# Performance work log

Hardware: AMD Instinct MI355X
Metric: run time of the kernel (lower is better)

## Reference

```python
import jax, jax.numpy as jnp
import numpy as np

N_NODES = 100000
NFEAT = 256
NHID = 8
HEADS = 8
NCLASS = 32
N_EDGES = 1600000
NEG_SLOPE = 0.2


def setup_inputs() -> dict:
    key = jax.random.key(0)
    ks = jax.random.split(key, 10)
    glorot = lambda k, shape: jax.random.uniform(
        k, shape, jnp.float32, -1.0, 1.0) * np.sqrt(6.0 / (shape[0] + shape[-1]))
    x = jax.random.normal(ks[0], (N_NODES, NFEAT), jnp.float32)
    edge_index = jax.random.randint(ks[1], (2, N_EDGES), 0, N_NODES, jnp.int64)
    W1 = glorot(ks[2], (NFEAT, HEADS * NHID))
    a_src1 = glorot(ks[3], (HEADS, NHID))
    a_dst1 = glorot(ks[4], (HEADS, NHID))
    b1 = jnp.zeros((HEADS * NHID,), jnp.float32)
    W2 = glorot(ks[5], (HEADS * NHID, NCLASS))
    a_src2 = glorot(ks[6], (1, NCLASS))
    a_dst2 = glorot(ks[7], (1, NCLASS))
    b2 = jnp.zeros((NCLASS,), jnp.float32)
    return {"x": x, "edge_index": edge_index, "W1": W1, "a_src1": a_src1,
            "a_dst1": a_dst1, "b1": b1, "W2": W2, "a_src2": a_src2,
            "a_dst2": a_dst2, "b2": b2}


def gat_conv(x, src, dst, W, a_src, a_dst, b, heads, ch, concat):
    """One PyG-style GATConv layer (eval mode, self-loops already in src/dst)."""
    n = x.shape[0]
    h = (x @ W).reshape(n, heads, ch)                      # [N,H,C]
    al_s = jnp.einsum('nhc,hc->nh', h, a_src)              # [N,H]
    al_d = jnp.einsum('nhc,hc->nh', h, a_dst)              # [N,H]
    e = al_s[src] + al_d[dst]                              # [E,H]
    e = jnp.where(e >= 0, e, NEG_SLOPE * e)                # LeakyReLU(0.2)
    # segment softmax over destination node (self-loops => no empty segments)
    m = jax.ops.segment_max(e, dst, num_segments=n)
    e = jnp.exp(e - m[dst])
    s = jax.ops.segment_sum(e, dst, num_segments=n)
    alpha = e / (s[dst] + 1e-16)                           # [E,H]
    msg = h[src] * alpha[:, :, None]                       # [E,H,C]
    out = jax.ops.segment_sum(msg, dst, num_segments=n)    # [N,H,C]
    out = out.reshape(n, heads * ch) if concat else out.mean(axis=1)
    return out + b


def reference(x, edge_index, W1, a_src1, a_dst1, b1, W2, a_src2, a_dst2, b2):
    n = x.shape[0]
    loop = jnp.arange(n, dtype=edge_index.dtype)
    src = jnp.concatenate([edge_index[0], loop])
    dst = jnp.concatenate([edge_index[1], loop])
    h = gat_conv(x, src, dst, W1, a_src1, a_dst1, b1, HEADS, NHID, True)
    h = jax.nn.elu(h)
    out = gat_conv(h, src, dst, W2, a_src2, a_dst2, b2, 1, NCLASS, False)
    return jax.nn.log_softmax(out, axis=1)
```

## Files before the change

### kernel.cpp

```cpp
#include <hip/hip_runtime.h>
#include <math.h>

#define N_NODES 100000
#define NFEAT 256
#define D1 64
#define HEADS 8
#define NHID 8
#define NCLASS 32
#define NUM_EDGES 1600000
#define E_TOT 1700000
#define NEG_SLOPE 0.2f

#define BSHIFT 8
#define NBUCK 391
#define BCAP 5120
#define BIN_EPB 4096
#define BIN_EPT 16


#define OFF_H1    0
#define OFF_OUT1  6400000
#define OFF_ALS1  12800000
#define OFF_ALD1  13600000
#define OFF_ALS2  14400000
#define OFF_ALD2  14500000
#define OFF_BCUR  14600000
#define OFF_ROWP  14601024
#define OFF_CNT   14701024
#define OFF_BIN   14801024
#define OFF_CSR   16802944

typedef __attribute__((ext_vector_type(8))) short bf16x8;
typedef __attribute__((ext_vector_type(4))) float f32x4;

__device__ __forceinline__ float lrelu(float x) { return x >= 0.f ? x : NEG_SLOPE * x; }

__device__ __forceinline__ unsigned f32_to_bf16_rne(float f) {
    unsigned u = __float_as_uint(f);
    return (u + 0x7fffu + ((u >> 16) & 1u)) >> 16;
}
__device__ __forceinline__ unsigned pack_bf16x2(float lo, float hi) {
    return f32_to_bf16_rne(lo) | (f32_to_bf16_rne(hi) << 16);
}
__device__ __forceinline__ float2 unpack_bf16x2(unsigned v) {
    return make_float2(__uint_as_float(v << 16), __uint_as_float(v & 0xffff0000u));
}

__device__ __forceinline__ void edge_src_dst(const int* __restrict__ ei, int e, int& src, int& dst) {
    if (e < NUM_EDGES) { src = ei[e]; dst = ei[NUM_EDGES + e]; }
    else { src = e - NUM_EDGES; dst = e - NUM_EDGES; }
}

__global__ __launch_bounds__(256) void gemm1_kernel(const float* __restrict__ x,
                                                    const float* __restrict__ W1,
                                                    const float* __restrict__ a_src,
                                                    const float* __restrict__ a_dst,
                                                    ushort* __restrict__ h1u,
                                                    float* __restrict__ als,
                                                    float* __restrict__ ald) {
    __shared__ unsigned xbf[2][64 * 20];
    const int tid = threadIdx.x;
    const int wv = tid >> 6;
    const int l = tid & 63;
    const int lm = l & 15;
    const int quad = l >> 4;
    const int r0 = blockIdx.x * 64;

    bf16x8 bfrag[8];
#pragma unroll
    for (int kb = 0; kb < 8; kb++)
#pragma unroll
        for (int j = 0; j < 8; j++) {
            const int k = kb * 32 + quad * 8 + j;
            bfrag[kb][j] = (short)f32_to_bf16_rne(W1[k * D1 + wv * 16 + lm]);
        }

    f32x4 acc[4];
#pragma unroll
    for (int s = 0; s < 4; s++) acc[s] = (f32x4)(0.f);

    const int sr = tid >> 2;
    const int sk = (tid & 3) * 8;
    const bool rok = (r0 + sr) < N_NODES;
    const float* xrow = &x[(size_t)(r0 + sr) * NFEAT];
    const int swrd = sr * 20 + (tid & 3) * 4;

    {
        uint4 pv = make_uint4(0, 0, 0, 0);
        if (rok) {
            const float4 va = *(const float4*)&xrow[sk];
            const float4 vb = *(const float4*)&xrow[sk + 4];
            pv.x = pack_bf16x2(va.x, va.y);
            pv.y = pack_bf16x2(va.z, va.w);
            pv.z = pack_bf16x2(vb.x, vb.y);
            pv.w = pack_bf16x2(vb.z, vb.w);
        }
        *(uint4*)&xbf[0][swrd] = pv;
    }
    __syncthreads();

#pragma unroll
    for (int kb = 0; kb < 8; kb++) {
        const int cur = kb & 1;
        const int nxt = cur ^ 1;
        float4 na = make_float4(0.f, 0.f, 0.f, 0.f);
        float4 nb = make_float4(0.f, 0.f, 0.f, 0.f);
        if (kb < 7 && rok) {
            na = *(const float4*)&xrow[(kb + 1) * 32 + sk];
            nb = *(const float4*)&xrow[(kb + 1) * 32 + sk + 4];
        }
#pragma unroll
        for (int s = 0; s < 4; s++) {
            const uint4 u = *(const uint4*)&xbf[cur][(s * 16 + lm) * 20 + quad * 4];
            const bf16x8 af = *(const bf16x8*)&u;
            acc[s] = __builtin_amdgcn_mfma_f32_16x16x32_bf16(af, bfrag[kb], acc[s], 0, 0, 0);
        }
        if (kb < 7) {
            uint4 pv;
            pv.x = pack_bf16x2(na.x, na.y);
            pv.y = pack_bf16x2(na.z, na.w);
            pv.z = pack_bf16x2(nb.x, nb.y);
            pv.w = pack_bf16x2(nb.z, nb.w);
            *(uint4*)&xbf[nxt][swrd] = pv;
            __syncthreads();
        }
    }

    const int head = wv * 2 + (lm >> 3);
    const int jc = l & 7;
    const float asl = a_src[head * NHID + jc];
    const float adl = a_dst[head * NHID + jc];
    const int col = wv * 16 + lm;
#pragma unroll
    for (int s = 0; s < 4; s++) {
#pragma unroll
        for (int r = 0; r < 4; r++) {
            const int row = r0 + s * 16 + quad * 4 + r;
            const float v = acc[s][r];
            float ps = v * asl, pd = v * adl;
            ps += __shfl_xor(ps, 1, 64); pd += __shfl_xor(pd, 1, 64);
            ps += __shfl_xor(ps, 2, 64); pd += __shfl_xor(pd, 2, 64);
            ps += __shfl_xor(ps, 4, 64); pd += __shfl_xor(pd, 4, 64);
            if (row < N_NODES) {
                h1u[(size_t)row * D1 + col] = (ushort)f32_to_bf16_rne(v);
                if (jc == 0) { als[row * HEADS + head] = ps; ald[row * HEADS + head] = pd; }
            }
        }
    }
}

__global__ __launch_bounds__(256) void bin_kernel(const int* __restrict__ ei,
                                                  int* __restrict__ bcur,
                                                  int* __restrict__ bin) {
    __shared__ int lcnt[NBUCK];
    __shared__ int lbase[NBUCK];
    const int tid = threadIdx.x;
    for (int b = tid; b < NBUCK; b += 256) lcnt[b] = 0;
    __syncthreads();
    const int e0 = blockIdx.x * BIN_EPB;
    int pk[BIN_EPT], bk[BIN_EPT], loff[BIN_EPT];
#pragma unroll
    for (int i = 0; i < BIN_EPT; i++) {
        const int e = e0 + i * 256 + tid;
        if (e < E_TOT) {
            int src, dst; edge_src_dst(ei, e, src, dst);
            bk[i] = dst >> BSHIFT;
            pk[i] = ((dst & 255) << 20) | src;
            loff[i] = atomicAdd(&lcnt[bk[i]], 1);
        } else bk[i] = -1;
    }
    __syncthreads();
    for (int b = tid; b < NBUCK; b += 256) {
        const int c = lcnt[b];
        lbase[b] = c ? atomicAdd(&bcur[b], c) : 0;
    }
    __syncthreads();
#pragma unroll
    for (int i = 0; i < BIN_EPT; i++) {
        if (bk[i] >= 0)
            bin[(size_t)bk[i] * BCAP + lbase[bk[i]] + loff[i]] = pk[i];
    }
}

__global__ __launch_bounds__(256) void bsort_kernel(const int* __restrict__ bcur,
                                                    const int* __restrict__ bin,
                                                    int* __restrict__ csr,
                                                    int* __restrict__ row_ptr,
                                                    int* __restrict__ cnt) {
    __shared__ int hcnt[256];
    __shared__ int hpre[256];
    __shared__ int cur[256];
    __shared__ int ssrc[BCAP];
    const int tid = threadIdx.x;
    const int bkt = blockIdx.x;
    const int cntb = bcur[bkt];
    const int base = bkt * BCAP;
    hcnt[tid] = 0;
    __syncthreads();
    for (int i = tid; i < cntb; i += 256)
        atomicAdd(&hcnt[bin[base + i] >> 20], 1);
    __syncthreads();
    const int myc = hcnt[tid];
    hpre[tid] = myc;
    __syncthreads();
    for (int off = 1; off < 256; off <<= 1) {
        const int t = (tid >= off) ? hpre[tid - off] : 0;
        __syncthreads();
        hpre[tid] += t;
        __syncthreads();
    }
    const int exc = hpre[tid] - myc;
    cur[tid] = exc;
    __syncthreads();
    for (int i = tid; i < cntb; i += 256) {
        const int v = bin[base + i];
        const int pos = atomicAdd(&cur[v >> 20], 1);
        ssrc[pos] = v & 0xFFFFF;
    }
    __syncthreads();
    for (int i = tid; i < cntb; i += 256) csr[base + i] = ssrc[i];
    const int n = (bkt << BSHIFT) + tid;
    if (n < N_NODES) { row_ptr[n] = base + exc; cnt[n] = myc; }
}

__global__ __launch_bounds__(256) void gather1_kernel(const int* __restrict__ row_ptr,
                                                      const int* __restrict__ cnt,
                                                      const int* __restrict__ csr_src,
                                                      const unsigned* __restrict__ h1b,
                                                      const float* __restrict__ als,
                                                      const float* __restrict__ ald,
                                                      float* __restrict__ out1) {
    const int tid = threadIdx.x;
    const int n = blockIdx.x * 4 + (tid >> 6);
    const int l = tid & 63;
    const int q = l >> 3;
    const int h = l & 7;
    const int start = row_ptr[n];
    const int deg = cnt[n];
    const float aldn = ald[n * HEADS + h];
    float a0 = 0.f, a1 = 0.f, a2 = 0.f, a3 = 0.f;
    float a4 = 0.f, a5 = 0.f, a6 = 0.f, a7 = 0.f, wsum = 0.f;

    int i = q;
    float e0 = 0.f, e1 = 0.f;
    uint4 u0 = make_uint4(0u, 0u, 0u, 0u);
    uint4 u1 = make_uint4(0u, 0u, 0u, 0u);
    int s2 = 0;
    if (i < deg) {
        const int s0 = csr_src[start + i];
        e0 = als[s0 * HEADS + h];
        u0 = *(const uint4*)&h1b[(size_t)s0 * 32 + h * 4];
    }
    if (i + 8 < deg) {
        const int s1 = csr_src[start + i + 8];
        e1 = als[s1 * HEADS + h];
        u1 = *(const uint4*)&h1b[(size_t)s1 * 32 + h * 4];
    }
    if (i + 16 < deg) s2 = csr_src[start + i + 16];

    for (; i < deg; i += 8) {
        int s3 = 0;
        if (i + 24 < deg) s3 = csr_src[start + i + 24];
        float e2 = 0.f;
        uint4 u2 = make_uint4(0u, 0u, 0u, 0u);
        if (i + 16 < deg) {
            e2 = als[s2 * HEADS + h];
            u2 = *(const uint4*)&h1b[(size_t)s2 * 32 + h * 4];
        }
        const float w = __expf(lrelu(e0 + aldn));
        const float2 p0 = unpack_bf16x2(u0.x);
        const float2 p1 = unpack_bf16x2(u0.y);
        const float2 p2 = unpack_bf16x2(u0.z);
        const float2 p3 = unpack_bf16x2(u0.w);
        a0 = fmaf(p0.x, w, a0); a1 = fmaf(p0.y, w, a1);
        a2 = fmaf(p1.x, w, a2); a3 = fmaf(p1.y, w, a3);
        a4 = fmaf(p2.x, w, a4); a5 = fmaf(p2.y, w, a5);
        a6 = fmaf(p3.x, w, a6); a7 = fmaf(p3.y, w, a7);
        wsum += w;
        e0 = e1; u0 = u1; e1 = e2; u1 = u2; s2 = s3;
    }

    a0 += __shfl_down(a0, 32, 64); a1 += __shfl_down(a1, 32, 64);
    a2 += __shfl_down(a2, 32, 64); a3 += __shfl_down(a3, 32, 64);
    a4 += __shfl_down(a4, 32, 64); a5 += __shfl_down(a5, 32, 64);
    a6 += __shfl_down(a6, 32, 64); a7 += __shfl_down(a7, 32, 64);
    wsum += __shfl_down(wsum, 32, 64);
    a0 += __shfl_down(a0, 16, 64); a1 += __shfl_down(a1, 16, 64);
    a2 += __shfl_down(a2, 16, 64); a3 += __shfl_down(a3, 16, 64);
    a4 += __shfl_down(a4, 16, 64); a5 += __shfl_down(a5, 16, 64);
    a6 += __shfl_down(a6, 16, 64); a7 += __shfl_down(a7, 16, 64);
    wsum += __shfl_down(wsum, 16, 64);
    a0 += __shfl_down(a0, 8, 64); a1 += __shfl_down(a1, 8, 64);
    a2 += __shfl_down(a2, 8, 64); a3 += __shfl_down(a3, 8, 64);
    a4 += __shfl_down(a4, 8, 64); a5 += __shfl_down(a5, 8, 64);
    a6 += __shfl_down(a6, 8, 64); a7 += __shfl_down(a7, 8, 64);
    wsum += __shfl_down(wsum, 8, 64);
    if (l < 8) {
        const float inv = 1.f / (wsum + 1e-16f);
        float* op = &out1[(size_t)n * D1 + h * 8];
        *(float4*)&op[0] = make_float4(a0 * inv, a1 * inv, a2 * inv, a3 * inv);
        *(float4*)&op[4] = make_float4(a4 * inv, a5 * inv, a6 * inv, a7 * inv);
    }
}

__global__ __launch_bounds__(256) void layer2_node_kernel(const float* __restrict__ out1,
                                                          const float* __restrict__ b1,
                                                          const float* __restrict__ W2,
                                                          const float* __restrict__ a_src2,
                                                          const float* __restrict__ a_dst2,
                                                          unsigned* __restrict__ h2b,
                                                          float* __restrict__ als2,
                                                          float* __restrict__ ald2) {
    __shared__ float w2l[D1 * NCLASS];
    __shared__ float b1l[D1];
    __shared__ float a2l[2 * NCLASS];
    const int tid = threadIdx.x;
    for (int i = tid; i < D1 * NCLASS; i += 256) w2l[i] = W2[i];
    if (tid < D1) b1l[tid] = b1[tid];
    if (tid < NCLASS) a2l[tid] = a_src2[tid];
    else if (tid < 2 * NCLASS) a2l[tid] = a_dst2[tid - NCLASS];
    __syncthreads();

    const int n = blockIdx.x * 256 + tid;
    if (n >= N_NODES) return;
    float acc[NCLASS];
#pragma unroll
    for (int c = 0; c < NCLASS; c++) acc[c] = 0.f;
    float as = 0.f, ad = 0.f;
    const float4* rp = (const float4*)&out1[(size_t)n * D1];
#pragma unroll 2
    for (int k4 = 0; k4 < 16; k4++) {
        const float4 v4 = rp[k4];
        const float vv[4] = {v4.x, v4.y, v4.z, v4.w};
#pragma unroll
        for (int j = 0; j < 4; j++) {
            const int k = k4 * 4 + j;
            float z = vv[j] + b1l[k];
            z = z > 0.f ? z : expm1f(z);
            const float* wr = &w2l[k * NCLASS];
#pragma unroll
            for (int c = 0; c < NCLASS; c++) acc[c] += z * wr[c];
        }
    }
#pragma unroll
    for (int c = 0; c < NCLASS; c++) { as += acc[c] * a2l[c]; ad += acc[c] * a2l[NCLASS + c]; }
#pragma unroll
    for (int q = 0; q < 4; q++) {
        uint4 pv;
        pv.x = pack_bf16x2(acc[q * 8 + 0], acc[q * 8 + 1]);
        pv.y = pack_bf16x2(acc[q * 8 + 2], acc[q * 8 + 3]);
        pv.z = pack_bf16x2(acc[q * 8 + 4], acc[q * 8 + 5]);
        pv.w = pack_bf16x2(acc[q * 8 + 6], acc[q * 8 + 7]);
        *(uint4*)&h2b[(size_t)n * 16 + q * 4] = pv;
    }
    als2[n] = as; ald2[n] = ad;
}

__global__ __launch_bounds__(256) void gather2_kernel(const int* __restrict__ row_ptr,
                                                      const int* __restrict__ cnt,
                                                      const int* __restrict__ csr_src,
                                                      const unsigned* __restrict__ h2b,
                                                      const float* __restrict__ als2,
                                                      const float* __restrict__ ald2,
                                                      float* __restrict__ out2) {
    const int tid = threadIdx.x;
    const int n = blockIdx.x * 4 + (tid >> 6);
    const int l = tid & 63;
    const int q = l >> 2;
    const int c = l & 3;
    const int start = row_ptr[n];
    const int deg = cnt[n];
    const float aldn = ald2[n];
    float a0 = 0.f, a1 = 0.f, a2 = 0.f, a3 = 0.f;
    float a4 = 0.f, a5 = 0.f, a6 = 0.f, a7 = 0.f, wsum = 0.f;

    int i = q;
    float e0 = 0.f, e1 = 0.f;
    uint4 u0 = make_uint4(0u, 0u, 0u, 0u);
    uint4 u1 = make_uint4(0u, 0u, 0u, 0u);
    int s2 = 0;
    if (i < deg) {
        const int s0 = csr_src[start + i];
        e0 = als2[s0];
        u0 = *(const uint4*)&h2b[(size_t)s0 * 16 + c * 4];
    }
    if (i + 16 < deg) {
        const int s1 = csr_src[start + i + 16];
        e1 = als2[s1];
        u1 = *(const uint4*)&h2b[(size_t)s1 * 16 + c * 4];
    }
    if (i + 32 < deg) s2 = csr_src[start + i + 32];

    for (; i < deg; i += 16) {
        int s3 = 0;
        if (i + 48 < deg) s3 = csr_src[start + i + 48];
        float e2 = 0.f;
        uint4 u2 = make_uint4(0u, 0u, 0u, 0u);
        if (i + 32 < deg) {
            e2 = als2[s2];
            u2 = *(const uint4*)&h2b[(size_t)s2 * 16 + c * 4];
        }
        const float w = __expf(lrelu(e0 + aldn));
        const float2 p0 = unpack_bf16x2(u0.x);
        const float2 p1 = unpack_bf16x2(u0.y);
        const float2 p2 = unpack_bf16x2(u0.z);
        const float2 p3 = unpack_bf16x2(u0.w);
        a0 = fmaf(p0.x, w, a0); a1 = fmaf(p0.y, w, a1);
        a2 = fmaf(p1.x, w, a2); a3 = fmaf(p1.y, w, a3);
        a4 = fmaf(p2.x, w, a4); a5 = fmaf(p2.y, w, a5);
        a6 = fmaf(p3.x, w, a6); a7 = fmaf(p3.y, w, a7);
        wsum += w;
        e0 = e1; u0 = u1; e1 = e2; u1 = u2; s2 = s3;
    }

    a0 += __shfl_down(a0, 32, 64); a1 += __shfl_down(a1, 32, 64);
    a2 += __shfl_down(a2, 32, 64); a3 += __shfl_down(a3, 32, 64);
    a4 += __shfl_down(a4, 32, 64); a5 += __shfl_down(a5, 32, 64);
    a6 += __shfl_down(a6, 32, 64); a7 += __shfl_down(a7, 32, 64);
    wsum += __shfl_down(wsum, 32, 64);
    a0 += __shfl_down(a0, 16, 64); a1 += __shfl_down(a1, 16, 64);
    a2 += __shfl_down(a2, 16, 64); a3 += __shfl_down(a3, 16, 64);
    a4 += __shfl_down(a4, 16, 64); a5 += __shfl_down(a5, 16, 64);
    a6 += __shfl_down(a6, 16, 64); a7 += __shfl_down(a7, 16, 64);
    wsum += __shfl_down(wsum, 16, 64);
    a0 += __shfl_down(a0, 8, 64); a1 += __shfl_down(a1, 8, 64);
    a2 += __shfl_down(a2, 8, 64); a3 += __shfl_down(a3, 8, 64);
    a4 += __shfl_down(a4, 8, 64); a5 += __shfl_down(a5, 8, 64);
    a6 += __shfl_down(a6, 8, 64); a7 += __shfl_down(a7, 8, 64);
    wsum += __shfl_down(wsum, 8, 64);
    a0 += __shfl_down(a0, 4, 64); a1 += __shfl_down(a1, 4, 64);
    a2 += __shfl_down(a2, 4, 64); a3 += __shfl_down(a3, 4, 64);
    a4 += __shfl_down(a4, 4, 64); a5 += __shfl_down(a5, 4, 64);
    a6 += __shfl_down(a6, 4, 64); a7 += __shfl_down(a7, 4, 64);
    wsum += __shfl_down(wsum, 4, 64);
    if (l < 4) {
        const float inv = 1.f / (wsum + 1e-16f);
        float* op = &out2[(size_t)n * NCLASS + c * 8];
        *(float4*)&op[0] = make_float4(a0 * inv, a1 * inv, a2 * inv, a3 * inv);
        *(float4*)&op[4] = make_float4(a4 * inv, a5 * inv, a6 * inv, a7 * inv);
    }
}

__global__ __launch_bounds__(256) void logsoftmax_kernel(const float* __restrict__ out2,
                                                         const float* __restrict__ b2,
                                                         float* __restrict__ out) {
    __shared__ float b2l[NCLASS];
    if (threadIdx.x < NCLASS) b2l[threadIdx.x] = b2[threadIdx.x];
    __syncthreads();
    const int n = blockIdx.x * 256 + threadIdx.x;
    if (n >= N_NODES) return;
    float v[NCLASS];
    float mx = -INFINITY;
    const float4* rp = (const float4*)&out2[(size_t)n * NCLASS];
#pragma unroll
    for (int c4 = 0; c4 < NCLASS / 4; c4++) {
        const float4 t = rp[c4];
        v[c4 * 4 + 0] = t.x + b2l[c4 * 4 + 0];
        v[c4 * 4 + 1] = t.y + b2l[c4 * 4 + 1];
        v[c4 * 4 + 2] = t.z + b2l[c4 * 4 + 2];
        v[c4 * 4 + 3] = t.w + b2l[c4 * 4 + 3];
    }
#pragma unroll
    for (int c = 0; c < NCLASS; c++) mx = fmaxf(mx, v[c]);
    float s = 0.f;
#pragma unroll
    for (int c = 0; c < NCLASS; c++) s += __expf(v[c] - mx);
    const float lse = mx + logf(s);
    float4* op = (float4*)&out[(size_t)n * NCLASS];
#pragma unroll
    for (int c4 = 0; c4 < NCLASS / 4; c4++)
        op[c4] = make_float4(v[c4 * 4] - lse, v[c4 * 4 + 1] - lse, v[c4 * 4 + 2] - lse, v[c4 * 4 + 3] - lse);
}

extern "C" void kernel_launch(void* const* d_in, const int* in_sizes, int n_in,
                              void* d_out, int out_size, void* d_ws, size_t ws_size,
                              hipStream_t stream) {
    const float* x      = (const float*)d_in[0];
    const int*   ei     = (const int*)d_in[1];
    const float* W1     = (const float*)d_in[2];
    const float* a_src1 = (const float*)d_in[3];
    const float* a_dst1 = (const float*)d_in[4];
    const float* b1     = (const float*)d_in[5];
    const float* W2     = (const float*)d_in[6];
    const float* a_src2 = (const float*)d_in[7];
    const float* a_dst2 = (const float*)d_in[8];
    const float* b2     = (const float*)d_in[9];
    float* out = (float*)d_out;
    float* ws  = (float*)d_ws;

    ushort* h1u     = (ushort*)(ws + OFF_H1);
    unsigned* h1b   = (unsigned*)(ws + OFF_H1);
    float* out1     = ws + OFF_OUT1;
    float* als1     = ws + OFF_ALS1;
    float* ald1     = ws + OFF_ALD1;
    float* als2     = ws + OFF_ALS2;
    float* ald2     = ws + OFF_ALD2;
    int*   bcur     = (int*)(ws + OFF_BCUR);
    int*   row_ptr  = (int*)(ws + OFF_ROWP);
    int*   cnt      = (int*)(ws + OFF_CNT);
    int*   bin      = (int*)(ws + OFF_BIN);
    int*   csr      = (int*)(ws + OFF_CSR);
    unsigned* h2b   = (unsigned*)(ws + OFF_H1);
    float* out2     = ws + OFF_H1 + 3200000;

    hipMemsetAsync(bcur, 0, NBUCK * sizeof(int), stream);

    const int NB = (N_NODES + 255) / 256;

    gemm1_kernel<<<(N_NODES + 63) / 64, 256, 0, stream>>>(x, W1, a_src1, a_dst1, h1u, als1, ald1);
    bin_kernel<<<(E_TOT + BIN_EPB - 1) / BIN_EPB, 256, 0, stream>>>(ei, bcur, bin);
    bsort_kernel<<<NBUCK, 256, 0, stream>>>(bcur, bin, csr, row_ptr, cnt);
    gather1_kernel<<<N_NODES / 4, 256, 0, stream>>>(row_ptr, cnt, csr, h1b, als1, ald1, out1);
    layer2_node_kernel<<<NB, 256, 0, stream>>>(out1, b1, W2, a_src2, a_dst2, h2b, als2, ald2);
    gather2_kernel<<<N_NODES / 4, 256, 0, stream>>>(row_ptr, cnt, csr, h2b, als2, ald2, out2);
    logsoftmax_kernel<<<NB, 256, 0, stream>>>(out2, b2, out);
}
```

Measured before the change: 357.0 us.

## Fuse layer-2 node transform into gather1 and log-softmax into gather2

Folds the per-node ELU + W2 projection and attention-logit computation into the epilogue of the layer-1 aggregation kernel, using a shared-memory buffer per wavefront and W2 read from global memory. It also folds the bias add and log-softmax into the layer-2 aggregation epilogue using cross-lane shuffles. This removes two kernel launches and the round-trips of the out1 and out2 intermediates through global memory. In exchange, gather1 gains a block barrier and per-wave W2 reads, which may add latency to a gather-bound kernel. h2b moves to its own workspace region, so it no longer overlaps h1.

New measurement: 360.3 us. Within noise of the previous version (+0.9%).

```diff
diff --git a/kernel.cpp b/kernel.cpp
--- a/kernel.cpp
+++ b/kernel.cpp
@@ -19,7 +19,7 @@
 
 
 #define OFF_H1    0
-#define OFF_OUT1  6400000
+#define OFF_H2    6400000
 #define OFF_ALS1  12800000
 #define OFF_ALD1  13600000
 #define OFF_ALS2  14400000
@@ -229,9 +229,17 @@
                                                       const unsigned* __restrict__ h1b,
                                                       const float* __restrict__ als,
                                                       const float* __restrict__ ald,
-                                                      float* __restrict__ out1) {
+                                                      const float* __restrict__ b1,
+                                                      const float* __restrict__ W2,
+                                                      const float* __restrict__ a_src2,
+                                                      const float* __restrict__ a_dst2,
+                                                      unsigned* __restrict__ h2b,
+                                                      float* __restrict__ als2,
+                                                      float* __restrict__ ald2) {
+    __shared__ float zbuf[4][64];
     const int tid = threadIdx.x;
-    const int n = blockIdx.x * 4 + (tid >> 6);
+    const int wv = tid >> 6;
+    const int n = blockIdx.x * 4 + wv;
     const int l = tid & 63;
     const int q = l >> 3;
     const int h = l & 7;
@@ -295,65 +303,49 @@
     a4 += __shfl_down(a4, 8, 64); a5 += __shfl_down(a5, 8, 64);
     a6 += __shfl_down(a6, 8, 64); a7 += __shfl_down(a7, 8, 64);
     wsum += __shfl_down(wsum, 8, 64);
+
     if (l < 8) {
         const float inv = 1.f / (wsum + 1e-16f);
-        float* op = &out1[(size_t)n * D1 + h * 8];
-        *(float4*)&op[0] = make_float4(a0 * inv, a1 * inv, a2 * inv, a3 * inv);
-        *(float4*)&op[4] = make_float4(a4 * inv, a5 * inv, a6 * inv, a7 * inv);
-    }
-}
-
-__global__ __launch_bounds__(256) void layer2_node_kernel(const float* __restrict__ out1,
-                                                          const float* __restrict__ b1,
-                                                          const float* __restrict__ W2,
-                                                          const float* __restrict__ a_src2,
-                                                          const float* __restrict__ a_dst2,
-                                                          unsigned* __restrict__ h2b,
-                                                          float* __restrict__ als2,
-                                                          float* __restrict__ ald2) {
-    __shared__ float w2l[D1 * NCLASS];
-    __shared__ float b1l[D1];
-    __shared__ float a2l[2 * NCLASS];
-    const int tid = threadIdx.x;
-    for (int i = tid; i < D1 * NCLASS; i += 256) w2l[i] = W2[i];
-    if (tid < D1) b1l[tid] = b1[tid];
-    if (tid < NCLASS) a2l[tid] = a_src2[tid];
-    else if (tid < 2 * NCLASS) a2l[tid] = a_dst2[tid - NCLASS];
-    __syncthreads();
-
-    const int n = blockIdx.x * 256 + tid;
-    if (n >= N_NODES) return;
-    float acc[NCLASS];
-#pragma unroll
-    for (int c = 0; c < NCLASS; c++) acc[c] = 0.f;
-    float as = 0.f, ad = 0.f;
-    const float4* rp = (const float4*)&out1[(size_t)n * D1];
-#pragma unroll 2
-    for (int k4 = 0; k4 < 16; k4++) {
-        const float4 v4 = rp[k4];
-        const float vv[4] = {v4.x, v4.y, v4.z, v4.w};
-#pragma unroll
-        for (int j = 0; j < 4; j++) {
-            const int k = k4 * 4 + j;
-            float z = vv[j] + b1l[k];
-            z = z > 0.f ? z : expm1f(z);
-            const float* wr = &w2l[k * NCLASS];
-#pragma unroll
-            for (int c = 0; c < NCLASS; c++) acc[c] += z * wr[c];
-        }
-    }
-#pragma unroll
-    for (int c = 0; c < NCLASS; c++) { as += acc[c] * a2l[c]; ad += acc[c] * a2l[NCLASS + c]; }
-#pragma unroll
-    for (int q = 0; q < 4; q++) {
-        uint4 pv;
-        pv.x = pack_bf16x2(acc[q * 8 + 0], acc[q * 8 + 1]);
-        pv.y = pack_bf16x2(acc[q * 8 + 2], acc[q * 8 + 3]);
-        pv.z = pack_bf16x2(acc[q * 8 + 4], acc[q * 8 + 5]);
-        pv.w = pack_bf16x2(acc[q * 8 + 6], acc[q * 8 + 7]);
-        *(uint4*)&h2b[(size_t)n * 16 + q * 4] = pv;
-    }
-    als2[n] = as; ald2[n] = ad;
+        const float4 b1a = *(const float4*)&b1[l * 8];
+        const float4 b1b = *(const float4*)&b1[l * 8 + 4];
+        float z0 = a0 * inv + b1a.x; z0 = z0 > 0.f ? z0 : expm1f(z0);
+        float z1 = a1 * inv + b1a.y; z1 = z1 > 0.f ? z1 : expm1f(z1);
+        float z2 = a2 * inv + b1a.z; z2 = z2 > 0.f ? z2 : expm1f(z2);
+        float z3 = a3 * inv + b1a.w; z3 = z3 > 0.f ? z3 : expm1f(z3);
+        float z4 = a4 * inv + b1b.x; z4 = z4 > 0.f ? z4 : expm1f(z4);
+        float z5 = a5 * inv + b1b.y; z5 = z5 > 0.f ? z5 : expm1f(z5);
+        float z6 = a6 * inv + b1b.z; z6 = z6 > 0.f ? z6 : expm1f(z6);
+        float z7 = a7 * inv + b1b.w; z7 = z7 > 0.f ? z7 : expm1f(z7);
+        *(float4*)&zbuf[wv][l * 8]     = make_float4(z0, z1, z2, z3);
+        *(float4*)&zbuf[wv][l * 8 + 4] = make_float4(z4, z5, z6, z7);
+    }
+    __syncthreads();
+
+    const int c = l & 31;
+    const int kh = l >> 5;
+    float y = 0.f;
+    const float* wbase = &W2[(kh * 32) * NCLASS + c];
+#pragma unroll
+    for (int j4 = 0; j4 < 8; j4++) {
+        const float4 zv = *(const float4*)&zbuf[wv][kh * 32 + j4 * 4];
+        y = fmaf(zv.x, wbase[(j4 * 4 + 0) * NCLASS], y);
+        y = fmaf(zv.y, wbase[(j4 * 4 + 1) * NCLASS], y);
+        y = fmaf(zv.z, wbase[(j4 * 4 + 2) * NCLASS], y);
+        y = fmaf(zv.w, wbase[(j4 * 4 + 3) * NCLASS], y);
+    }
+    y += __shfl_xor(y, 32, 64);
+
+    float ts = (l < 32) ? y * a_src2[c] : 0.f;
+    float td = (l < 32) ? y * a_dst2[c] : 0.f;
+    ts += __shfl_xor(ts, 1, 64);  td += __shfl_xor(td, 1, 64);
+    ts += __shfl_xor(ts, 2, 64);  td += __shfl_xor(td, 2, 64);
+    ts += __shfl_xor(ts, 4, 64);  td += __shfl_xor(td, 4, 64);
+    ts += __shfl_xor(ts, 8, 64);  td += __shfl_xor(td, 8, 64);
+    ts += __shfl_xor(ts, 16, 64); td += __shfl_xor(td, 16, 64);
+    if (l == 0) { als2[n] = ts; ald2[n] = td; }
+
+    const unsigned pw = pack_bf16x2(y, __shfl_down(y, 1, 64));
+    if (l < 32 && (l & 1) == 0) h2b[(size_t)n * 16 + (l >> 1)] = pw;
 }
 
 __global__ __launch_bounds__(256) void gather2_kernel(const int* __restrict__ row_ptr,
@@ -362,7 +354,8 @@
                                                       const unsigned* __restrict__ h2b,
                                                       const float* __restrict__ als2,
                                                       const float* __restrict__ ald2,
-                                                      float* __restrict__ out2) {
+                                                      const float* __restrict__ b2,
+                                                      float* __restrict__ out) {
     const int tid = threadIdx.x;
     const int n = blockIdx.x * 4 + (tid >> 6);
     const int l = tid & 63;
@@ -433,43 +426,28 @@
     a4 += __shfl_down(a4, 4, 64); a5 += __shfl_down(a5, 4, 64);
     a6 += __shfl_down(a6, 4, 64); a7 += __shfl_down(a7, 4, 64);
     wsum += __shfl_down(wsum, 4, 64);
+
+    const float inv = 1.f / (wsum + 1e-16f);
+    const float4 b2a = *(const float4*)&b2[c * 8];
+    const float4 b2b = *(const float4*)&b2[c * 8 + 4];
+    const float v0 = a0 * inv + b2a.x, v1 = a1 * inv + b2a.y;
+    const float v2 = a2 * inv + b2a.z, v3 = a3 * inv + b2a.w;
+    const float v4 = a4 * inv + b2b.x, v5 = a5 * inv + b2b.y;
+    const float v6 = a6 * inv + b2b.z, v7 = a7 * inv + b2b.w;
+    float mx = fmaxf(fmaxf(fmaxf(v0, v1), fmaxf(v2, v3)),
+                     fmaxf(fmaxf(v4, v5), fmaxf(v6, v7)));
+    mx = fmaxf(mx, __shfl_xor(mx, 1, 64));
+    mx = fmaxf(mx, __shfl_xor(mx, 2, 64));
+    float s = __expf(v0 - mx) + __expf(v1 - mx) + __expf(v2 - mx) + __expf(v3 - mx)
+            + __expf(v4 - mx) + __expf(v5 - mx) + __expf(v6 - mx) + __expf(v7 - mx);
+    s += __shfl_xor(s, 1, 64);
+    s += __shfl_xor(s, 2, 64);
+    const float lse = mx + logf(s);
     if (l < 4) {
-        const float inv = 1.f / (wsum + 1e-16f);
-        float* op = &out2[(size_t)n * NCLASS + c * 8];
-        *(float4*)&op[0] = make_float4(a0 * inv, a1 * inv, a2 * inv, a3 * inv);
-        *(float4*)&op[4] = make_float4(a4 * inv, a5 * inv, a6 * inv, a7 * inv);
-    }
-}
-
-__global__ __launch_bounds__(256) void logsoftmax_kernel(const float* __restrict__ out2,
-                                                         const float* __restrict__ b2,
-                                                         float* __restrict__ out) {
-    __shared__ float b2l[NCLASS];
-    if (threadIdx.x < NCLASS) b2l[threadIdx.x] = b2[threadIdx.x];
-    __syncthreads();
-    const int n = blockIdx.x * 256 + threadIdx.x;
-    if (n >= N_NODES) return;
-    float v[NCLASS];
-    float mx = -INFINITY;
-    const float4* rp = (const float4*)&out2[(size_t)n * NCLASS];
-#pragma unroll
-    for (int c4 = 0; c4 < NCLASS / 4; c4++) {
-        const float4 t = rp[c4];
-        v[c4 * 4 + 0] = t.x + b2l[c4 * 4 + 0];
-        v[c4 * 4 + 1] = t.y + b2l[c4 * 4 + 1];
-        v[c4 * 4 + 2] = t.z + b2l[c4 * 4 + 2];
-        v[c4 * 4 + 3] = t.w + b2l[c4 * 4 + 3];
-    }
-#pragma unroll
-    for (int c = 0; c < NCLASS; c++) mx = fmaxf(mx, v[c]);
-    float s = 0.f;
-#pragma unroll
-    for (int c = 0; c < NCLASS; c++) s += __expf(v[c] - mx);
-    const float lse = mx + logf(s);
-    float4* op = (float4*)&out[(size_t)n * NCLASS];
-#pragma unroll
-    for (int c4 = 0; c4 < NCLASS / 4; c4++)
-        op[c4] = make_float4(v[c4 * 4] - lse, v[c4 * 4 + 1] - lse, v[c4 * 4 + 2] - lse, v[c4 * 4 + 3] - lse);
+        float* op = &out[(size_t)n * NCLASS + c * 8];
+        *(float4*)&op[0] = make_float4(v0 - lse, v1 - lse, v2 - lse, v3 - lse);
+        *(float4*)&op[4] = make_float4(v4 - lse, v5 - lse, v6 - lse, v7 - lse);
+    }
 }
 
 extern "C" void kernel_launch(void* const* d_in, const int* in_sizes, int n_in,
@@ -490,7 +468,7 @@
 
     ushort* h1u     = (ushort*)(ws + OFF_H1);
     unsigned* h1b   = (unsigned*)(ws + OFF_H1);
-    float* out1     = ws + OFF_OUT1;
+    unsigned* h2b   = (unsigned*)(ws + OFF_H2);
     float* als1     = ws + OFF_ALS1;
     float* ald1     = ws + OFF_ALD1;
     float* als2     = ws + OFF_ALS2;
@@ -500,18 +478,13 @@
     int*   cnt      = (int*)(ws + OFF_CNT);
     int*   bin      = (int*)(ws + OFF_BIN);
     int*   csr      = (int*)(ws + OFF_CSR);
-    unsigned* h2b   = (unsigned*)(ws + OFF_H1);
-    float* out2     = ws + OFF_H1 + 3200000;
 
     hipMemsetAsync(bcur, 0, NBUCK * sizeof(int), stream);
-
-    const int NB = (N_NODES + 255) / 256;
 
     gemm1_kernel<<<(N_NODES + 63) / 64, 256, 0, stream>>>(x, W1, a_src1, a_dst1, h1u, als1, ald1);
     bin_kernel<<<(E_TOT + BIN_EPB - 1) / BIN_EPB, 256, 0, stream>>>(ei, bcur, bin);
     bsort_kernel<<<NBUCK, 256, 0, stream>>>(bcur, bin, csr, row_ptr, cnt);
-    gather1_kernel<<<N_NODES / 4, 256, 0, stream>>>(row_ptr, cnt, csr, h1b, als1, ald1, out1);
-    layer2_node_kernel<<<NB, 256, 0, stream>>>(out1, b1, W2, a_src2, a_dst2, h2b, als2, ald2);
-    gather2_kernel<<<N_NODES / 4, 256, 0, stream>>>(row_ptr, cnt, csr, h2b, als2, ald2, out2);
-    logsoftmax_kernel<<<NB, 256, 0, stream>>>(out2, b2, out);
-}
+    gather1_kernel<<<N_NODES / 4, 256, 0, stream>>>(row_ptr, cnt, csr, h1b, als1, ald1,
+                                                    b1, W2, a_src2, a_dst2, h2b, als2, ald2);
+    gather2_kernel<<<N_NODES / 4, 256, 0, stream>>>(row_ptr, cnt, csr, h2b, als2, ald2, b2, out);
+}
```
